# Kernel optimization log

Measured on AMD Instinct MI355X. Metric: run time of the kernel, lower is better.

## Reference

```python
import jax, jax.numpy as jnp
import numpy as np

NUM_HEADS = 16
WINDOW = 64


def setup_inputs() -> dict:
    key = jax.random.key(0)
    ks = jax.random.split(key, 6)
    b, l, d = 2, 2048, 1024
    s = 1.0 / np.sqrt(d)
    return {
        "x": jax.random.normal(ks[0], (b, l, d), dtype=jnp.float32),
        "Wq": jax.random.normal(ks[1], (d, d), dtype=jnp.float32) * s,
        "Wk": jax.random.normal(ks[2], (d, d), dtype=jnp.float32) * s,
        "Wv": jax.random.normal(ks[3], (d, d), dtype=jnp.float32) * s,
        "Wo": jax.random.normal(ks[4], (d, d), dtype=jnp.float32) * s,
        "bo": jax.random.normal(ks[5], (d,), dtype=jnp.float32) * 0.01,
    }


def reference(x, Wq, Wk, Wv, Wo, bo):
    b, l, d = x.shape
    h, w = NUM_HEADS, WINDOW
    dh = d // h
    p = w // 2
    # Projections. Padding is zeros and proj_k/proj_v have no bias, so
    # padding-then-projecting equals projecting-then-zero-padding.
    q = (x @ Wq.T).reshape(b, l, h, dh)                     # (b,l,h,dh)
    xp = jnp.pad(x, ((0, 0), (p, p), (0, 0)))               # (b,l+2p,d)
    k = (xp @ Wk.T).reshape(b, l + 2 * p, h, dh)
    v = (xp @ Wv.T).reshape(b, l + 2 * p, h, dh)
    # Sliding windows: query i attends to padded positions i .. i+w-1
    win_idx = jnp.arange(l)[:, None] + jnp.arange(w)[None, :]  # (l,w)
    kw = k[:, win_idx]                                       # (b,l,w,h,dh)
    vw = v[:, win_idx]                                       # (b,l,w,h,dh)
    scale = 1.0 / np.float32(np.sqrt(dh))
    scores = jnp.einsum('blhd,blwhd->blhw', q, kw) * scale   # (b,l,h,w)
    attn = jax.nn.softmax(scores, axis=-1)
    out = jnp.einsum('blhw,blwhd->blhd', attn, vw).reshape(b, l, d)
    return out @ Wo.T + bo
```

## Files before the change

kernel.cpp:

```cpp
#include <hip/hip_runtime.h>
#include <hip/hip_bf16.h>
#include <cstdint>

typedef __bf16 bf16;
typedef __bf16 bf16x4 __attribute__((ext_vector_type(4)));
typedef __bf16 bf16x8 __attribute__((ext_vector_type(8)));
typedef float floatx4 __attribute__((ext_vector_type(4)));

typedef __attribute__((address_space(1))) void as1_void;
typedef __attribute__((address_space(3))) void as3_void;

__device__ __forceinline__ void gld16(const void* g, void* l) {
#if __has_builtin(__builtin_amdgcn_global_load_lds)
  __builtin_amdgcn_global_load_lds((as1_void*)(uintptr_t)g, (as3_void*)l, 16, 0, 0);
#else
  *(uint4*)l = *(const uint4*)g;
#endif
}

__global__ __launch_bounds__(256) void convert_kernel(
    const float* __restrict__ x, const float* __restrict__ wq,
    const float* __restrict__ wk, const float* __restrict__ wv,
    const float* __restrict__ wo, bf16* __restrict__ xbf,
    bf16* __restrict__ wqkv, bf16* __restrict__ wob) {
  int i = blockIdx.x * 256 + threadIdx.x;
  const float* src;
  bf16* dst;
  int off;
  if (i < 1048576) {
    src = x; dst = xbf; off = i;
  } else if (i < 1310720) {
    src = wq; dst = wqkv; off = i - 1048576;
  } else if (i < 1572864) {
    src = wk; dst = wqkv + 1048576; off = i - 1310720;
  } else if (i < 1835008) {
    src = wv; dst = wqkv + 2097152; off = i - 1572864;
  } else {
    src = wo; dst = wob; off = i - 1835008;
  }
  float4 v = ((const float4*)src)[off];
  bf16x4 o;
  o[0] = (bf16)v.x; o[1] = (bf16)v.y; o[2] = (bf16)v.z; o[3] = (bf16)v.w;
  ((bf16x4*)dst)[off] = o;
}

template <int MODE, int BN>
__global__ __launch_bounds__(256) void gemm_nt(const bf16* __restrict__ A,
                                               const bf16* __restrict__ Bm,
                                               bf16* __restrict__ Cb,
                                               float* __restrict__ Cf,
                                               const float* __restrict__ bias,
                                               int M, int N, int K) {
  constexpr int WN = BN / 2;
  constexpr int NI = WN / 16;
  __shared__ __attribute__((aligned(16))) bf16 As[128 * 32];
  __shared__ __attribute__((aligned(16))) bf16 Bs[BN * 32];
  const int tid = threadIdx.x;
  const int lane = tid & 63;
  const int wave = tid >> 6;
  const int quad = lane >> 4;
  const int n0 = lane & 15;
  const int wm = wave >> 1;
  const int wn = wave & 1;
  const int bN = blockIdx.x, bM = blockIdx.y;
  const bf16* Ab = A + (size_t)bM * 128 * K;
  const bf16* Bb = Bm + (size_t)bN * BN * K;
  const int c0 = tid, c1 = tid + 256;
  floatx4 acc[4][NI] = {};
  for (int k0 = 0; k0 < K; k0 += 32) {
    gld16(Ab + (size_t)(c0 >> 2) * K + k0 + (c0 & 3) * 8, &As[c0 * 8]);
    gld16(Ab + (size_t)(c1 >> 2) * K + k0 + (c1 & 3) * 8, &As[c1 * 8]);
#pragma unroll
    for (int cc = 0; cc < BN * 4; cc += 256) {
      const int c = cc + tid;
      gld16(Bb + (size_t)(c >> 2) * K + k0 + (c & 3) * 8, &Bs[c * 8]);
    }
    __syncthreads();
    bf16x8 af[4], bfr[NI];
#pragma unroll
    for (int mi = 0; mi < 4; ++mi)
      af[mi] = *(const bf16x8*)&As[(wm * 64 + mi * 16 + n0) * 32 + quad * 8];
#pragma unroll
    for (int ni = 0; ni < NI; ++ni)
      bfr[ni] = *(const bf16x8*)&Bs[(wn * WN + ni * 16 + n0) * 32 + quad * 8];
#pragma unroll
    for (int mi = 0; mi < 4; ++mi)
#pragma unroll
      for (int ni = 0; ni < NI; ++ni)
        acc[mi][ni] = __builtin_amdgcn_mfma_f32_16x16x32_bf16(
            af[mi], bfr[ni], acc[mi][ni], 0, 0, 0);
    __syncthreads();
  }
  const int rowBase = bM * 128 + wm * 64;
  const int colBase = bN * BN + wn * WN;
#pragma unroll
  for (int ni = 0; ni < NI; ++ni) {
    const int col = colBase + ni * 16 + n0;
    float badd = 0.f;
    if (MODE == 1) badd = bias[col];
#pragma unroll
    for (int mi = 0; mi < 4; ++mi)
#pragma unroll
      for (int r = 0; r < 4; ++r) {
        const int row = rowBase + mi * 16 + quad * 4 + r;
        if (MODE == 0)
          Cb[(size_t)row * N + col] = (bf16)acc[mi][ni][r];
        else
          Cf[(size_t)row * N + col] = acc[mi][ni][r] + badd;
      }
  }
}

__global__ __launch_bounds__(256) void attn_kernel(const bf16* __restrict__ qkv,
                                                   bf16* __restrict__ aout) {
  __shared__ __attribute__((aligned(16))) bf16 Ks[128 * 72];
  __shared__ __attribute__((aligned(16))) bf16 VsPs[128 * 72];
  __shared__ __attribute__((aligned(16))) bf16 Vt[64 * 136];
  const int bid = blockIdx.x;
  const int b = bid >> 9;
  const int h = (bid >> 5) & 15;
  const int i0 = (bid & 31) * 64;
  const int tid = threadIdx.x;
  const int wave = tid >> 6, lane = tid & 63;
  const int quad = lane >> 4, n0 = lane & 15;
  bf16* Vs = VsPs;

#pragma unroll
  for (int it = 0; it < 4; ++it) {
    const int idx = it * 256 + tid;
    const int r = idx >> 3, c = idx & 7;
    const int j = i0 - 32 + r;
    uint4 kv_ = make_uint4(0u, 0u, 0u, 0u);
    uint4 vv = make_uint4(0u, 0u, 0u, 0u);
    if (j >= 0 && j < 2048) {
      const bf16* base = qkv + (size_t)(b * 2048 + j) * 3072 + 1024 + h * 64 + c * 8;
      kv_ = *(const uint4*)base;
      vv = *(const uint4*)(base + 1024);
    }
    *(uint4*)&Ks[r * 72 + c * 8] = kv_;
    *(uint4*)&Vs[r * 72 + c * 8] = vv;
  }
  __syncthreads();

#pragma unroll
  for (int it = 0; it < 4; ++it) {
    const int idx = it * 256 + tid;
    const int t = idx & 127, c = idx >> 7;
    bf16x8 v = *(const bf16x8*)&Vs[t * 72 + c * 8];
#pragma unroll
    for (int jj = 0; jj < 8; ++jj) Vt[(c * 8 + jj) * 136 + t] = v[jj];
  }
  __syncthreads();

  bf16x8 aq[2];
#pragma unroll
  for (int ks = 0; ks < 2; ++ks)
    aq[ks] = *(const bf16x8*)(qkv +
        (size_t)(b * 2048 + i0 + wave * 16 + n0) * 3072 + h * 64 + ks * 32 + quad * 8);

  floatx4 accS[8] = {};
#pragma unroll
  for (int nt = 0; nt < 8; ++nt)
#pragma unroll
    for (int ks = 0; ks < 2; ++ks) {
      bf16x8 bk = *(const bf16x8*)&Ks[(nt * 16 + n0) * 72 + ks * 32 + quad * 8];
      accS[nt] = __builtin_amdgcn_mfma_f32_16x16x32_bf16(aq[ks], bk, accS[nt], 0, 0, 0);
    }

  float mrow[4] = {-1e30f, -1e30f, -1e30f, -1e30f};
#pragma unroll
  for (int nt = 0; nt < 8; ++nt)
#pragma unroll
    for (int r = 0; r < 4; ++r) {
      const int q64 = wave * 16 + quad * 4 + r;
      const int t = nt * 16 + n0;
      float s = accS[nt][r] * 0.125f;
      if (t < q64 || t >= q64 + 64) s = -1e30f;
      accS[nt][r] = s;
      mrow[r] = fmaxf(mrow[r], s);
    }
#pragma unroll
  for (int off = 1; off < 16; off <<= 1)
#pragma unroll
    for (int r = 0; r < 4; ++r)
      mrow[r] = fmaxf(mrow[r], __shfl_xor(mrow[r], off));
  float lrow[4] = {0.f, 0.f, 0.f, 0.f};
#pragma unroll
  for (int nt = 0; nt < 8; ++nt)
#pragma unroll
    for (int r = 0; r < 4; ++r) {
      const float e = __expf(accS[nt][r] - mrow[r]);
      accS[nt][r] = e;
      lrow[r] += e;
    }
#pragma unroll
  for (int off = 1; off < 16; off <<= 1)
#pragma unroll
    for (int r = 0; r < 4; ++r) lrow[r] += __shfl_xor(lrow[r], off);

  bf16* Pw = &VsPs[wave * 16 * 136];
#pragma unroll
  for (int r = 0; r < 4; ++r) {
    const float inv = 1.f / lrow[r];
#pragma unroll
    for (int nt = 0; nt < 8; ++nt)
      Pw[(quad * 4 + r) * 136 + nt * 16 + n0] = (bf16)(accS[nt][r] * inv);
  }

  floatx4 accO[4] = {};
#pragma unroll
  for (int kt = 0; kt < 4; ++kt) {
    bf16x8 ap = *(const bf16x8*)&Pw[n0 * 136 + kt * 32 + quad * 8];
#pragma unroll
    for (int dt = 0; dt < 4; ++dt) {
      bf16x8 bv = *(const bf16x8*)&Vt[(dt * 16 + n0) * 136 + kt * 32 + quad * 8];
      accO[dt] = __builtin_amdgcn_mfma_f32_16x16x32_bf16(ap, bv, accO[dt], 0, 0, 0);
    }
  }
#pragma unroll
  for (int dt = 0; dt < 4; ++dt)
#pragma unroll
    for (int r = 0; r < 4; ++r) {
      const int q64 = wave * 16 + quad * 4 + r;
      aout[(size_t)(b * 2048 + i0 + q64) * 1024 + h * 64 + dt * 16 + n0] =
          (bf16)accO[dt][r];
    }
}

extern "C" void kernel_launch(void* const* d_in, const int* in_sizes, int n_in,
                              void* d_out, int out_size, void* d_ws, size_t ws_size,
                              hipStream_t stream) {
  const float* x = (const float*)d_in[0];
  const float* wq = (const float*)d_in[1];
  const float* wk = (const float*)d_in[2];
  const float* wv = (const float*)d_in[3];
  const float* wo = (const float*)d_in[4];
  const float* bo = (const float*)d_in[5];
  char* ws = (char*)d_ws;
  bf16* xbf = (bf16*)(ws);
  bf16* wqkv = (bf16*)(ws + (8u << 20));
  bf16* wob = (bf16*)(ws + (14u << 20));
  bf16* qkv = (bf16*)(ws + (16u << 20));
  bf16* aout = xbf;

  convert_kernel<<<8192, 256, 0, stream>>>(x, wq, wk, wv, wo, xbf, wqkv, wob);
  gemm_nt<0, 128><<<dim3(24, 32), 256, 0, stream>>>(xbf, wqkv, qkv, nullptr,
                                                    nullptr, 4096, 3072, 1024);
  attn_kernel<<<1024, 256, 0, stream>>>(qkv, aout);
  gemm_nt<1, 64><<<dim3(16, 32), 256, 0, stream>>>(aout, wob, nullptr,
                                                   (float*)d_out, bo, 4096, 1024,
                                                   1024);
}
```

Measured before the change: 157.8 us.

## Split-K output projection with 64-deep K tiles and separate bias reduction

The GEMM main loop now stages a 64-wide K slab per iteration, two 32-wide sub-slabs, which halves the number of barrier pairs. The output projection switches from BN=64 to BN=128 tiles and splits K across two z-slices, writing fp32 partials to workspace. A new reduce kernel sums the two partials and adds the bias. This keeps 512 blocks on the output GEMM with larger tiles, at the cost of extra partial-sum memory traffic and one more launch.

```diff
diff --git a/kernel.cpp b/kernel.cpp
--- a/kernel.cpp
+++ b/kernel.cpp
@@ -49,12 +49,11 @@
                                                const bf16* __restrict__ Bm,
                                                bf16* __restrict__ Cb,
                                                float* __restrict__ Cf,
-                                               const float* __restrict__ bias,
                                                int M, int N, int K) {
   constexpr int WN = BN / 2;
   constexpr int NI = WN / 16;
-  __shared__ __attribute__((aligned(16))) bf16 As[128 * 32];
-  __shared__ __attribute__((aligned(16))) bf16 Bs[BN * 32];
+  __shared__ __attribute__((aligned(16))) bf16 As[2 * 128 * 32];
+  __shared__ __attribute__((aligned(16))) bf16 Bs[2 * BN * 32];
   const int tid = threadIdx.x;
   const int lane = tid & 63;
   const int wave = tid >> 6;
@@ -62,42 +61,50 @@
   const int n0 = lane & 15;
   const int wm = wave >> 1;
   const int wn = wave & 1;
-  const int bN = blockIdx.x, bM = blockIdx.y;
+  const int bN = blockIdx.x, bM = blockIdx.y, bZ = blockIdx.z;
+  const int Kslice = K / gridDim.z;
+  const int kBeg = bZ * Kslice;
   const bf16* Ab = A + (size_t)bM * 128 * K;
   const bf16* Bb = Bm + (size_t)bN * BN * K;
-  const int c0 = tid, c1 = tid + 256;
   floatx4 acc[4][NI] = {};
-  for (int k0 = 0; k0 < K; k0 += 32) {
-    gld16(Ab + (size_t)(c0 >> 2) * K + k0 + (c0 & 3) * 8, &As[c0 * 8]);
-    gld16(Ab + (size_t)(c1 >> 2) * K + k0 + (c1 & 3) * 8, &As[c1 * 8]);
-#pragma unroll
-    for (int cc = 0; cc < BN * 4; cc += 256) {
+  for (int k0 = kBeg; k0 < kBeg + Kslice; k0 += 64) {
+#pragma unroll
+    for (int it = 0; it < 4; ++it) {
+      const int c = it * 256 + tid;
+      const int slab = c >> 9, rk = c & 511, row = rk >> 2, kq = rk & 3;
+      gld16(Ab + (size_t)row * K + k0 + slab * 32 + kq * 8, &As[c * 8]);
+    }
+#pragma unroll
+    for (int cc = 0; cc < BN * 8; cc += 256) {
       const int c = cc + tid;
-      gld16(Bb + (size_t)(c >> 2) * K + k0 + (c & 3) * 8, &Bs[c * 8]);
+      const int slab = c / (BN * 4), rk = c % (BN * 4), row = rk >> 2, kq = rk & 3;
+      gld16(Bb + (size_t)row * K + k0 + slab * 32 + kq * 8, &Bs[c * 8]);
     }
     __syncthreads();
-    bf16x8 af[4], bfr[NI];
-#pragma unroll
-    for (int mi = 0; mi < 4; ++mi)
-      af[mi] = *(const bf16x8*)&As[(wm * 64 + mi * 16 + n0) * 32 + quad * 8];
-#pragma unroll
-    for (int ni = 0; ni < NI; ++ni)
-      bfr[ni] = *(const bf16x8*)&Bs[(wn * WN + ni * 16 + n0) * 32 + quad * 8];
-#pragma unroll
-    for (int mi = 0; mi < 4; ++mi)
+#pragma unroll
+    for (int ks = 0; ks < 2; ++ks) {
+      bf16x8 af[4], bfr[NI];
+#pragma unroll
+      for (int mi = 0; mi < 4; ++mi)
+        af[mi] = *(const bf16x8*)&As[ks * 4096 + (wm * 64 + mi * 16 + n0) * 32 + quad * 8];
 #pragma unroll
       for (int ni = 0; ni < NI; ++ni)
-        acc[mi][ni] = __builtin_amdgcn_mfma_f32_16x16x32_bf16(
-            af[mi], bfr[ni], acc[mi][ni], 0, 0, 0);
+        bfr[ni] = *(const bf16x8*)&Bs[ks * BN * 32 + (wn * WN + ni * 16 + n0) * 32 + quad * 8];
+#pragma unroll
+      for (int mi = 0; mi < 4; ++mi)
+#pragma unroll
+        for (int ni = 0; ni < NI; ++ni)
+          acc[mi][ni] = __builtin_amdgcn_mfma_f32_16x16x32_bf16(
+              af[mi], bfr[ni], acc[mi][ni], 0, 0, 0);
+    }
     __syncthreads();
   }
   const int rowBase = bM * 128 + wm * 64;
   const int colBase = bN * BN + wn * WN;
+  float* Cfp = Cf + (size_t)bZ * M * N;
 #pragma unroll
   for (int ni = 0; ni < NI; ++ni) {
     const int col = colBase + ni * 16 + n0;
-    float badd = 0.f;
-    if (MODE == 1) badd = bias[col];
 #pragma unroll
     for (int mi = 0; mi < 4; ++mi)
 #pragma unroll
@@ -106,9 +113,24 @@
         if (MODE == 0)
           Cb[(size_t)row * N + col] = (bf16)acc[mi][ni][r];
         else
-          Cf[(size_t)row * N + col] = acc[mi][ni][r] + badd;
+          Cfp[(size_t)row * N + col] = acc[mi][ni][r];
       }
   }
+}
+
+__global__ __launch_bounds__(256) void reduce_bias_kernel(
+    const float* __restrict__ p, const float* __restrict__ bias,
+    float* __restrict__ out) {
+  const int i = blockIdx.x * 256 + threadIdx.x;
+  float4 a = ((const float4*)p)[i];
+  float4 c = ((const float4*)(p + 4194304))[i];
+  float4 bi = ((const float4*)bias)[i & 255];
+  float4 o;
+  o.x = a.x + c.x + bi.x;
+  o.y = a.y + c.y + bi.y;
+  o.z = a.z + c.z + bi.z;
+  o.w = a.w + c.w + bi.w;
+  ((float4*)out)[i] = o;
 }
 
 __global__ __launch_bounds__(256) void attn_kernel(const bf16* __restrict__ qkv,
@@ -241,13 +263,14 @@
   bf16* wqkv = (bf16*)(ws + (8u << 20));
   bf16* wob = (bf16*)(ws + (14u << 20));
   bf16* qkv = (bf16*)(ws + (16u << 20));
+  float* part = (float*)(ws + (40u << 20));
   bf16* aout = xbf;
 
   convert_kernel<<<8192, 256, 0, stream>>>(x, wq, wk, wv, wo, xbf, wqkv, wob);
-  gemm_nt<0, 128><<<dim3(24, 32), 256, 0, stream>>>(xbf, wqkv, qkv, nullptr,
-                                                    nullptr, 4096, 3072, 1024);
+  gemm_nt<0, 128><<<dim3(24, 32, 1), 256, 0, stream>>>(xbf, wqkv, qkv, nullptr,
+                                                       4096, 3072, 1024);
   attn_kernel<<<1024, 256, 0, stream>>>(qkv, aout);
-  gemm_nt<1, 64><<<dim3(16, 32), 256, 0, stream>>>(aout, wob, nullptr,
-                                                   (float*)d_out, bo, 4096, 1024,
-                                                   1024);
-}
+  gemm_nt<1, 128><<<dim3(8, 32, 2), 256, 0, stream>>>(aout, wob, nullptr, part,
+                                                      4096, 1024, 1024);
+  reduce_bias_kernel<<<4096, 256, 0, stream>>>(part, bo, (float*)d_out);
+}
```

New measurement: 158.5 us. About the same (+0.4%).
